# Kernel optimization log

Measured on AMD Instinct MI355X. Metric: run time of the kernel, lower is better.

The kernel has to match this reference:

```python
import jax, jax.numpy as jnp
import numpy as np

B, T, V, D = 8, 256, 32, 256


def setup_inputs() -> dict:
    key = jax.random.key(0)
    k1, k2 = jax.random.split(key)
    # scale by 0.1 so exp(q.k) stays well within fp32 range (dot std ~ 0.1^2*sqrt(D))
    feature = jax.random.normal(k1, (B, T, V, D), dtype=jnp.float32) * 0.1
    feature_aug = jax.random.normal(k2, (B, T, V, D), dtype=jnp.float32) * 0.1
    return {"feature": feature, "feature_aug": feature_aug}


def reference(feature, feature_aug):
    # match torch permute(0,2,1,3): [B,T,V,D] -> [B,V,T,D]
    f = jnp.transpose(feature, (0, 2, 1, 3))      # [B,V,Tq,D]
    fa = jnp.transpose(feature_aug, (0, 2, 1, 3))  # [B,V,Tk,D]
    # all-pairs QK^T scores: [B_i, B_j, V, Tq, Tk]
    scores = jnp.einsum('ivqd,jvkd->ijvqk', f, fa)
    E = jnp.exp(scores)
    # positive (j == i): ap = exp(scores[i,i]).sum over V, Tq -> [B, Tk]
    diag = jnp.einsum('iivqk->ivqk', E)           # [B,V,Tq,Tk]
    ap_exp = diag.sum(axis=(1, 2))                # [B, Tk]
    # negatives (j != i): sum over j,V,Tk minus the j==i part -> [B, Tq]
    total = E.sum(axis=(1, 2, 4))                 # [B, Tq]
    self_part = diag.sum(axis=(1, 3))             # [B, Tq]
    an_exp = total - self_part                    # [B, Tq]
    # per-anchor loss vector [T]; original sums over anchors then takes .mean()
    loss_vec = -jnp.log(ap_exp / an_exp)          # [B, T]
    return loss_vec.sum(axis=0).mean()
```

## Files before the change

### kernel.cpp

```cpp
#include <hip/hip_runtime.h>
#include <hip/hip_bf16.h>


typedef __attribute__((ext_vector_type(4))) float f32x4;
typedef __attribute__((ext_vector_type(4))) int   i32x4;
typedef __attribute__((ext_vector_type(8))) int   i32x8;
typedef __attribute__((ext_vector_type(8))) __bf16 bf16x8;

#if __has_builtin(__builtin_amdgcn_exp2f)
#define EXP2(x) __builtin_amdgcn_exp2f(x)
#else
#define EXP2(x) exp2f(x)
#endif

#define WAIT_VMCNT(N)                                              \
    do {                                                           \
        asm volatile("s_waitcnt vmcnt(" #N ")" ::: "memory");      \
        __builtin_amdgcn_sched_barrier(0);                         \
    } while (0)
#define WAIT_LGKM0                                                 \
    do {                                                           \
        asm volatile("s_waitcnt lgkmcnt(0)" ::: "memory");         \
        __builtin_amdgcn_sched_barrier(0);                         \
    } while (0)
#define BARRIER()                                                  \
    do {                                                           \
        __builtin_amdgcn_s_barrier();                              \
        __builtin_amdgcn_sched_barrier(0);                         \
    } while (0)

__device__ __forceinline__ unsigned short f2bf(float f) {
    unsigned u = __builtin_bit_cast(unsigned, f);
    u += 0x7FFFu + ((u >> 16) & 1u);
    return (unsigned short)(u >> 16);
}

template <bool HI>
__device__ __forceinline__ unsigned cvt2fp8(float a, float b, unsigned old) {
    return __builtin_amdgcn_cvt_pk_fp8_f32(a, b, old, HI);
}
__device__ __forceinline__ unsigned pack4fp8(float x, float y, float z, float w) {
    return cvt2fp8<true>(z, w, cvt2fp8<false>(x, y, 0u));
}

__device__ __forceinline__ void async16(const void* g, void* l) {
    __builtin_amdgcn_global_load_lds(
        (const __attribute__((address_space(1))) unsigned int*)g,
        (__attribute__((address_space(3))) unsigned int*)l,
        16, 0, 0);
}

__device__ __forceinline__ i32x8 cat8(i32x4 lo, i32x4 hi) {
    i32x8 r;
    r[0] = lo[0]; r[1] = lo[1]; r[2] = lo[2]; r[3] = lo[3];
    r[4] = hi[0]; r[5] = hi[1]; r[6] = hi[2]; r[7] = hi[3];
    return r;
}

template <int CTRL>
__device__ __forceinline__ float dpp_add(float x) {
    int y = __builtin_amdgcn_update_dpp(0, __builtin_bit_cast(int, x),
                                        CTRL, 0xf, 0xf, true);
    return x + __builtin_bit_cast(float, y);
}
__device__ __forceinline__ float rowsum16(float x) {
    x = dpp_add<0x111>(x);
    x = dpp_add<0x112>(x);
    x = dpp_add<0x114>(x);
    x = dpp_add<0x118>(x);
    return x;
}

__global__ __launch_bounds__(256) void infonce_repack_fp8(
    const float* __restrict__ feat, const float* __restrict__ feat_aug,
    unsigned char* __restrict__ pA, unsigned char* __restrict__ pB,
    float* __restrict__ counters)
{
    const int tid = threadIdx.x;
    if (blockIdx.x == 0 && blockIdx.y == 0) {
        #pragma unroll
        for (int k = 0; k < 24; ++k) counters[k * 256 + tid] = 0.f;
    }
    const bool isA = (blockIdx.y == 0);
    const float sc = isA ? 1.4426950408889634f : 1.0f;
    const float* src = isA ? feat : feat_aug;
    unsigned char* dst = isA ? pA : pB;
    const unsigned g = blockIdx.x * 256u + (unsigned)tid;
    #pragma unroll
    for (int it = 0; it < 8; ++it) {
        const unsigned idx = it * 524288u + g;
        const float4 f = *(const float4*)(src + (size_t)idx * 4);
        const unsigned p = pack4fp8(f.x * sc, f.y * sc, f.z * sc, f.w * sc);
        *(unsigned*)(dst + (size_t)idx * 4) = p;
    }
}

__global__ __launch_bounds__(256, 2) void infonce_main_nl(
    const unsigned char* __restrict__ pA, const unsigned char* __restrict__ pB,
    float* __restrict__ total, float* __restrict__ selfp, float* __restrict__ ap)
{
    __shared__ __align__(16) unsigned char As[128 * 256];
    __shared__ __align__(16) unsigned char Bs[2][64 * 256];
    float (*ls_row2)[128]  = (float (*)[128])(void*)As;
    float (*ls_self2)[128] = (float (*)[128])(void*)(As + 1024);

    const int tid  = threadIdx.x;
    const int lane = tid & 63;
    const int w    = tid >> 6;
    const int wm   = w >> 1;
    const int wn   = w & 1;
    const int lrow = lane & 15;
    const int quad = lane >> 4;

    const int tileM = blockIdx.x;
    const int v     = blockIdx.y;
    const int nD0   = (tileM >> 1) * 4;

    const size_t vOff = (size_t)v * 256;

    {
        const size_t rowM = (size_t)(tileM * 128 + w * 32 + quad) * 8192 + vOff;
        #pragma unroll
        for (int i = 0; i < 8; ++i) {
            const int lg = (lrow ^ ((i * 4 + quad) & 15)) << 4;
            async16(pA + rowM + (size_t)i * 4 * 8192 + lg, &As[(w * 32 + i * 4) * 256]);
        }
    }
    const size_t rowNbase = (size_t)(w * 16 + quad) * 8192 + vOff;
    #pragma unroll
    for (int nn = 0; nn < 2; ++nn) {
        const unsigned char* srcB = pB + rowNbase + (size_t)nn * 64 * 8192;
        #pragma unroll
        for (int i = 0; i < 4; ++i) {
            const int lg = (lrow ^ ((i * 4 + quad) & 15)) << 4;
            async16(srcB + (size_t)i * 4 * 8192 + lg,
                    &Bs[nn][(w * 16 + i * 4) * 256]);
        }
    }
    WAIT_VMCNT(4);
    BARRIER();

    i32x8 af[2][4];
    #pragma unroll
    for (int h = 0; h < 2; ++h)
        #pragma unroll
        for (int t = 0; t < 4; ++t) {
            const int rA = (wm * 64 + t * 16 + lrow) * 256;
            const int g0 = ((h * 8 + quad * 2) ^ lrow) * 16;
            af[h][t] = cat8(*(const i32x4*)&As[rA + g0],
                            *(const i32x4*)&As[rA + (g0 ^ 16)]);
        }

    float rowp[4][4];
    float selfr[4][4];
    #pragma unroll
    for (int t = 0; t < 4; ++t)
        #pragma unroll
        for (int r = 0; r < 4; ++r) { rowp[t][r] = 0.f; selfr[t][r] = 0.f; }

    auto iterBody = [&](const int n) {
        const int b = n & 1;
        BARRIER();

        i32x8 bfr[2][2];
        #pragma unroll
        for (int h = 0; h < 2; ++h)
            #pragma unroll
            for (int tj = 0; tj < 2; ++tj) {
                const int rB = (wn * 32 + tj * 16 + lrow) * 256;
                const int g0 = ((h * 8 + quad * 2) ^ lrow) * 16;
                bfr[h][tj] = cat8(*(const i32x4*)&Bs[b][rB + g0],
                                  *(const i32x4*)&Bs[b][rB + (g0 ^ 16)]);
            }
        WAIT_LGKM0;
        BARRIER();

        if (n < 30) {
            const unsigned char* src = pB + rowNbase + (size_t)(n + 2) * 64 * 8192;
            #pragma unroll
            for (int i = 0; i < 4; ++i) {
                const int lg = (lrow ^ ((i * 4 + quad) & 15)) << 4;
                async16(src + (size_t)i * 4 * 8192 + lg,
                        &Bs[b][(w * 16 + i * 4) * 256]);
            }
        }

        f32x4 acc[4][2];
        #pragma unroll
        for (int t = 0; t < 4; ++t)
            #pragma unroll
            for (int tj = 0; tj < 2; ++tj)
                acc[t][tj] = (f32x4){0.f, 0.f, 0.f, 0.f};
        __builtin_amdgcn_s_setprio(1);
        #pragma unroll
        for (int h = 0; h < 2; ++h)
            #pragma unroll
            for (int ti = 0; ti < 4; ++ti)
                #pragma unroll
                for (int tj = 0; tj < 2; ++tj)
                    acc[ti][tj] = __builtin_amdgcn_mfma_scale_f32_16x16x128_f8f6f4(
                        af[h][ti], bfr[h][tj], acc[ti][tj],
                        0, 0, 0, 127, 0, 127);
        __builtin_amdgcn_s_setprio(0);

        const bool diagIter = (n >= nD0) && (n < nD0 + 4);
        float colp0 = 0.f, colp1 = 0.f;
        #pragma unroll
        for (int t = 0; t < 4; ++t)
            #pragma unroll
            for (int r = 0; r < 4; ++r) {
                float e0 = EXP2(acc[t][0][r]);
                float e1 = EXP2(acc[t][1][r]);
                rowp[t][r] += e0 + e1;
                if (diagIter) { selfr[t][r] += e0 + e1; colp0 += e0; colp1 += e1; }
            }
        if (diagIter) {
            float q0 = colp0, q1 = colp1;
            q0 += __shfl_xor(q0, 16); q0 += __shfl_xor(q0, 32);
            q1 += __shfl_xor(q1, 16); q1 += __shfl_xor(q1, 32);
            if (lane < 16) {
                atomicAdd(&ap[n * 64 + wn * 32 + lane], q0);
                atomicAdd(&ap[n * 64 + wn * 32 + 16 + lane], q1);
            }
        }
    };

    for (int n = 0; n < 31; ++n) {
        WAIT_VMCNT(4);
        iterBody(n);
    }
    WAIT_VMCNT(0);
    iterBody(31);

    #pragma unroll
    for (int t = 0; t < 4; ++t)
        #pragma unroll
        for (int r = 0; r < 4; ++r) {
            float rs = rowsum16(rowp[t][r]);
            float ss = rowsum16(selfr[t][r]);
            if (lrow == 15) {
                const int idx = wm * 64 + t * 16 + quad * 4 + r;
                ls_row2[wn][idx]  = rs;
                ls_self2[wn][idx] = ss;
            }
        }
    __syncthreads();
    if (tid < 128) {
        atomicAdd(&total[tileM * 128 + tid], ls_row2[0][tid] + ls_row2[1][tid]);
    } else {
        const int t2 = tid - 128;
        atomicAdd(&selfp[tileM * 128 + t2], ls_self2[0][t2] + ls_self2[1][t2]);
    }
}

__global__ __launch_bounds__(256) void infonce_main_slow(
    const float* __restrict__ feat, const float* __restrict__ feat_aug,
    float* __restrict__ total, float* __restrict__ selfp, float* __restrict__ ap)
{
    __shared__ __align__(16) unsigned short As[128][72];
    __shared__ __align__(16) unsigned short Bs[128][72];
    __shared__ float ls_row[128];
    __shared__ float ls_col[128];

    const int tid  = threadIdx.x;
    const int lane = tid & 63;
    const int w    = tid >> 6;
    const int wm   = w >> 1;
    const int wn   = w & 1;
    const int lrow = lane & 15;
    const int quad = lane >> 4;

    const int tileM = blockIdx.x & 15;
    const int tileN = blockIdx.x >> 4;
    const int v     = blockIdx.y;
    const bool diag = (tileM >> 1) == (tileN >> 1);

    if (tid < 128) ls_row[tid] = 0.0f;
    else           ls_col[tid - 128] = 0.0f;

    const float* aBase = feat     + (size_t)v * 256;
    const float* bBase = feat_aug + (size_t)v * 256;

    f32x4 acc[4][4];
    #pragma unroll
    for (int i = 0; i < 4; ++i)
        #pragma unroll
        for (int j = 0; j < 4; ++j)
            acc[i][j] = (f32x4){0.f, 0.f, 0.f, 0.f};

    const int srow = tid >> 4;
    const int scol = (tid & 15) * 4;

    for (int s = 0; s < 4; ++s) {
        const int k0 = s * 64;
        if (s) __syncthreads();
        #pragma unroll
        for (int it = 0; it < 8; ++it) {
            const int row = it * 16 + srow;
            const float4 a4 = *(const float4*)(aBase + (size_t)(tileM * 128 + row) * 8192 + k0 + scol);
            const float4 b4 = *(const float4*)(bBase + (size_t)(tileN * 128 + row) * 8192 + k0 + scol);
            uint2 wa, wb;
            wa.x = (unsigned)f2bf(a4.x) | ((unsigned)f2bf(a4.y) << 16);
            wa.y = (unsigned)f2bf(a4.z) | ((unsigned)f2bf(a4.w) << 16);
            wb.x = (unsigned)f2bf(b4.x) | ((unsigned)f2bf(b4.y) << 16);
            wb.y = (unsigned)f2bf(b4.z) | ((unsigned)f2bf(b4.w) << 16);
            *(uint2*)&As[row][scol] = wa;
            *(uint2*)&Bs[row][scol] = wb;
        }
        __syncthreads();
        #pragma unroll
        for (int kk = 0; kk < 64; kk += 32) {
            bf16x8 af[4], bfr[4];
            #pragma unroll
            for (int t = 0; t < 4; ++t) {
                af[t]  = *(const bf16x8*)&As[wm * 64 + t * 16 + lrow][kk + quad * 8];
                bfr[t] = *(const bf16x8*)&Bs[wn * 64 + t * 16 + lrow][kk + quad * 8];
            }
            #pragma unroll
            for (int ti = 0; ti < 4; ++ti)
                #pragma unroll
                for (int tj = 0; tj < 4; ++tj)
                    acc[ti][tj] = __builtin_amdgcn_mfma_f32_16x16x32_bf16(
                        af[ti], bfr[tj], acc[ti][tj], 0, 0, 0);
        }
    }

    float colp[4] = {0.f, 0.f, 0.f, 0.f};
    #pragma unroll
    for (int ti = 0; ti < 4; ++ti) {
        #pragma unroll
        for (int r = 0; r < 4; ++r) {
            float e0 = __expf(acc[ti][0][r]);
            float e1 = __expf(acc[ti][1][r]);
            float e2 = __expf(acc[ti][2][r]);
            float e3 = __expf(acc[ti][3][r]);
            colp[0] += e0; colp[1] += e1; colp[2] += e2; colp[3] += e3;
            float rp = (e0 + e1) + (e2 + e3);
            rp += __shfl_xor(rp, 1);
            rp += __shfl_xor(rp, 2);
            rp += __shfl_xor(rp, 4);
            rp += __shfl_xor(rp, 8);
            if (lrow == 0)
                atomicAdd(&ls_row[wm * 64 + ti * 16 + quad * 4 + r], rp);
        }
    }
    if (diag) {
        #pragma unroll
        for (int tj = 0; tj < 4; ++tj) {
            float q = colp[tj];
            q += __shfl_xor(q, 16);
            q += __shfl_xor(q, 32);
            if (lane < 16)
                atomicAdd(&ls_col[wn * 64 + tj * 16 + lane], q);
        }
    }
    __syncthreads();
    if (tid < 128) {
        const float rs = ls_row[tid];
        const int rowg = tileM * 128 + tid;
        atomicAdd(&total[rowg], rs);
        if (diag) atomicAdd(&selfp[rowg], rs);
    } else if (diag) {
        const int t2 = tid - 128;
        atomicAdd(&ap[tileN * 128 + t2], ls_col[t2]);
    }
}

__global__ __launch_bounds__(256) void infonce_finalize(
    const float* __restrict__ total, const float* __restrict__ selfp,
    const float* __restrict__ ap, float* __restrict__ out)
{
    __shared__ float red[4];
    const int tid = threadIdx.x;
    float s = 0.f;
    for (int e = tid; e < 2048; e += 256) {
        const float an = total[e] - selfp[e];
        s += logf(an / ap[e]);
    }
    #pragma unroll
    for (int m = 32; m >= 1; m >>= 1) s += __shfl_xor(s, m);
    if ((tid & 63) == 0) red[tid >> 6] = s;
    __syncthreads();
    if (tid == 0) out[0] = (red[0] + red[1] + red[2] + red[3]) * (1.0f / 256.0f);
}

extern "C" void kernel_launch(void* const* d_in, const int* in_sizes, int n_in,
                              void* d_out, int out_size, void* d_ws, size_t ws_size,
                              hipStream_t stream) {
    const float* feat     = (const float*)d_in[0];
    const float* feat_aug = (const float*)d_in[1];
    float* total = (float*)d_ws;
    float* selfp = total + 2048;
    float* ap    = selfp + 2048;

    const size_t packBytes = (size_t)2048 * 8192;
    const size_t need = 32768 + 2 * packBytes;
    if (ws_size >= need) {
        unsigned char* pA = (unsigned char*)d_ws + 32768;
        unsigned char* pB = pA + packBytes;
        infonce_repack_fp8<<<dim3(2048, 2), 256, 0, stream>>>(feat, feat_aug, pA, pB, total);
        infonce_main_nl<<<dim3(16, 32), 256, 0, stream>>>(pA, pB, total, selfp, ap);
    } else {
        (void)hipMemsetAsync(d_ws, 0, 3 * 2048 * sizeof(float), stream);
        infonce_main_slow<<<dim3(256, 32), 256, 0, stream>>>(feat, feat_aug, total, selfp, ap);
    }
    infonce_finalize<<<1, 256, 0, stream>>>(total, selfp, ap, (float*)d_out);
}
```

Before: 189.2 us.

## Software-pipeline exp epilogue one iteration behind MFMA via ping-pong accumulators

```diff
diff --git a/kernel.cpp b/kernel.cpp
--- a/kernel.cpp
+++ b/kernel.cpp
@@ -158,8 +158,34 @@
         #pragma unroll
         for (int r = 0; r < 4; ++r) { rowp[t][r] = 0.f; selfr[t][r] = 0.f; }
 
-    auto iterBody = [&](const int n) {
+    f32x4 accA[4][2], accB[4][2];
+
+    auto epilogue = [&](const int m, f32x4 (&prev)[4][2]) {
+        const bool diagIter = (m >= nD0) && (m < nD0 + 4);
+        float colp0 = 0.f, colp1 = 0.f;
+        #pragma unroll
+        for (int t = 0; t < 4; ++t)
+            #pragma unroll
+            for (int r = 0; r < 4; ++r) {
+                float e0 = EXP2(prev[t][0][r]);
+                float e1 = EXP2(prev[t][1][r]);
+                rowp[t][r] += e0 + e1;
+                if (diagIter) { selfr[t][r] += e0 + e1; colp0 += e0; colp1 += e1; }
+            }
+        if (diagIter) {
+            float q0 = colp0, q1 = colp1;
+            q0 += __shfl_xor(q0, 16); q0 += __shfl_xor(q0, 32);
+            q1 += __shfl_xor(q1, 16); q1 += __shfl_xor(q1, 32);
+            if (lane < 16) {
+                atomicAdd(&ap[m * 64 + wn * 32 + lane], q0);
+                atomicAdd(&ap[m * 64 + wn * 32 + 16 + lane], q1);
+            }
+        }
+    };
+
+    auto step = [&](const int n, f32x4 (&cur)[4][2], f32x4 (&prev)[4][2]) {
         const int b = n & 1;
+        if (n == 31) { WAIT_VMCNT(0); } else { WAIT_VMCNT(4); }
         BARRIER();
 
         i32x8 bfr[2][2];
@@ -185,12 +211,11 @@
             }
         }
 
-        f32x4 acc[4][2];
         #pragma unroll
         for (int t = 0; t < 4; ++t)
             #pragma unroll
             for (int tj = 0; tj < 2; ++tj)
-                acc[t][tj] = (f32x4){0.f, 0.f, 0.f, 0.f};
+                cur[t][tj] = (f32x4){0.f, 0.f, 0.f, 0.f};
         __builtin_amdgcn_s_setprio(1);
         #pragma unroll
         for (int h = 0; h < 2; ++h)
@@ -198,39 +223,20 @@
             for (int ti = 0; ti < 4; ++ti)
                 #pragma unroll
                 for (int tj = 0; tj < 2; ++tj)
-                    acc[ti][tj] = __builtin_amdgcn_mfma_scale_f32_16x16x128_f8f6f4(
-                        af[h][ti], bfr[h][tj], acc[ti][tj],
+                    cur[ti][tj] = __builtin_amdgcn_mfma_scale_f32_16x16x128_f8f6f4(
+                        af[h][ti], bfr[h][tj], cur[ti][tj],
                         0, 0, 0, 127, 0, 127);
         __builtin_amdgcn_s_setprio(0);
 
-        const bool diagIter = (n >= nD0) && (n < nD0 + 4);
-        float colp0 = 0.f, colp1 = 0.f;
-        #pragma unroll
-        for (int t = 0; t < 4; ++t)
-            #pragma unroll
-            for (int r = 0; r < 4; ++r) {
-                float e0 = EXP2(acc[t][0][r]);
-                float e1 = EXP2(acc[t][1][r]);
-                rowp[t][r] += e0 + e1;
-                if (diagIter) { selfr[t][r] += e0 + e1; colp0 += e0; colp1 += e1; }
-            }
-        if (diagIter) {
-            float q0 = colp0, q1 = colp1;
-            q0 += __shfl_xor(q0, 16); q0 += __shfl_xor(q0, 32);
-            q1 += __shfl_xor(q1, 16); q1 += __shfl_xor(q1, 32);
-            if (lane < 16) {
-                atomicAdd(&ap[n * 64 + wn * 32 + lane], q0);
-                atomicAdd(&ap[n * 64 + wn * 32 + 16 + lane], q1);
-            }
-        }
+        if (n > 0) epilogue(n - 1, prev);
     };
 
-    for (int n = 0; n < 31; ++n) {
-        WAIT_VMCNT(4);
-        iterBody(n);
-    }
-    WAIT_VMCNT(0);
-    iterBody(31);
+    #pragma unroll 1
+    for (int hlf = 0; hlf < 16; ++hlf) {
+        step(2 * hlf,     accA, accB);
+        step(2 * hlf + 1, accB, accA);
+    }
+    epilogue(31, accB);
 
     #pragma unroll
     for (int t = 0; t < 4; ++t)
```

New measurement: 195.3 us. 1.03x slower.

## Fuse A-side fp8 conversion into main kernel, repack only feature_aug

Applied to the files above, without the earlier changes.

```diff
diff --git a/kernel.cpp b/kernel.cpp
--- a/kernel.cpp
+++ b/kernel.cpp
@@ -12,6 +12,8 @@
 #else
 #define EXP2(x) exp2f(x)
 #endif
+
+#define LOG2E 1.4426950408889634f
 
 #define WAIT_VMCNT(N)                                              \
     do {                                                           \
@@ -72,37 +74,32 @@
 }
 
 __global__ __launch_bounds__(256) void infonce_repack_fp8(
-    const float* __restrict__ feat, const float* __restrict__ feat_aug,
-    unsigned char* __restrict__ pA, unsigned char* __restrict__ pB,
+    const float* __restrict__ feat_aug, unsigned char* __restrict__ pB,
     float* __restrict__ counters)
 {
     const int tid = threadIdx.x;
-    if (blockIdx.x == 0 && blockIdx.y == 0) {
+    if (blockIdx.x == 0) {
         #pragma unroll
         for (int k = 0; k < 24; ++k) counters[k * 256 + tid] = 0.f;
     }
-    const bool isA = (blockIdx.y == 0);
-    const float sc = isA ? 1.4426950408889634f : 1.0f;
-    const float* src = isA ? feat : feat_aug;
-    unsigned char* dst = isA ? pA : pB;
     const unsigned g = blockIdx.x * 256u + (unsigned)tid;
     #pragma unroll
     for (int it = 0; it < 8; ++it) {
         const unsigned idx = it * 524288u + g;
-        const float4 f = *(const float4*)(src + (size_t)idx * 4);
-        const unsigned p = pack4fp8(f.x * sc, f.y * sc, f.z * sc, f.w * sc);
-        *(unsigned*)(dst + (size_t)idx * 4) = p;
+        const float4 f = *(const float4*)(feat_aug + (size_t)idx * 4);
+        const unsigned p = pack4fp8(f.x, f.y, f.z, f.w);
+        *(unsigned*)(pB + (size_t)idx * 4) = p;
     }
 }
 
 __global__ __launch_bounds__(256, 2) void infonce_main_nl(
-    const unsigned char* __restrict__ pA, const unsigned char* __restrict__ pB,
+    const float* __restrict__ feat, const unsigned char* __restrict__ pB,
     float* __restrict__ total, float* __restrict__ selfp, float* __restrict__ ap)
 {
-    __shared__ __align__(16) unsigned char As[128 * 256];
+    __shared__ __align__(16) unsigned char Stage[32 * 1024];
     __shared__ __align__(16) unsigned char Bs[2][64 * 256];
-    float (*ls_row2)[128]  = (float (*)[128])(void*)As;
-    float (*ls_self2)[128] = (float (*)[128])(void*)(As + 1024);
+    float (*ls_row2)[128]  = (float (*)[128])(void*)Stage;
+    float (*ls_self2)[128] = (float (*)[128])(void*)(Stage + 1024);
 
     const int tid  = threadIdx.x;
     const int lane = tid & 63;
@@ -118,14 +115,6 @@
 
     const size_t vOff = (size_t)v * 256;
 
-    {
-        const size_t rowM = (size_t)(tileM * 128 + w * 32 + quad) * 8192 + vOff;
-        #pragma unroll
-        for (int i = 0; i < 8; ++i) {
-            const int lg = (lrow ^ ((i * 4 + quad) & 15)) << 4;
-            async16(pA + rowM + (size_t)i * 4 * 8192 + lg, &As[(w * 32 + i * 4) * 256]);
-        }
-    }
     const size_t rowNbase = (size_t)(w * 16 + quad) * 8192 + vOff;
     #pragma unroll
     for (int nn = 0; nn < 2; ++nn) {
@@ -137,19 +126,44 @@
                     &Bs[nn][(w * 16 + i * 4) * 256]);
         }
     }
-    WAIT_VMCNT(4);
-    BARRIER();
 
     i32x8 af[2][4];
     #pragma unroll
-    for (int h = 0; h < 2; ++h)
-        #pragma unroll
-        for (int t = 0; t < 4; ++t) {
-            const int rA = (wm * 64 + t * 16 + lrow) * 256;
-            const int g0 = ((h * 8 + quad * 2) ^ lrow) * 16;
-            af[h][t] = cat8(*(const i32x4*)&As[rA + g0],
-                            *(const i32x4*)&As[rA + (g0 ^ 16)]);
-        }
+    for (int c = 0; c < 4; ++c) {
+        #pragma unroll
+        for (int i = 0; i < 8; ++i) {
+            const int rl = w * 8 + i;
+            const int gr = tileM * 128 + c * 32 + rl;
+            const int sg = lane ^ (rl & 15);
+            async16((const unsigned char*)feat +
+                        ((size_t)gr * 8192 + vOff + (size_t)sg * 4) * 4,
+                    &Stage[rl * 1024 + lane * 16]);
+        }
+        WAIT_VMCNT(0);
+        BARRIER();
+        if ((c >> 1) == wm) {
+            #pragma unroll
+            for (int tt = 0; tt < 2; ++tt) {
+                const int t  = (c & 1) * 2 + tt;
+                const int rl = tt * 16 + lrow;
+                #pragma unroll
+                for (int h = 0; h < 2; ++h) {
+                    i32x8 r;
+                    #pragma unroll
+                    for (int j = 0; j < 8; ++j) {
+                        const int G = h * 32 + quad * 8 + j;
+                        const float4 f = *(const float4*)
+                            &Stage[rl * 1024 + ((G ^ lrow) * 16)];
+                        r[j] = pack4fp8(f.x * LOG2E, f.y * LOG2E,
+                                        f.z * LOG2E, f.w * LOG2E);
+                    }
+                    af[h][t] = r;
+                }
+            }
+        }
+        WAIT_LGKM0;
+        BARRIER();
+    }
 
     float rowp[4][4];
     float selfr[4][4];
@@ -394,12 +408,11 @@
     float* ap    = selfp + 2048;
 
     const size_t packBytes = (size_t)2048 * 8192;
-    const size_t need = 32768 + 2 * packBytes;
+    const size_t need = 32768 + packBytes;
     if (ws_size >= need) {
-        unsigned char* pA = (unsigned char*)d_ws + 32768;
-        unsigned char* pB = pA + packBytes;
-        infonce_repack_fp8<<<dim3(2048, 2), 256, 0, stream>>>(feat, feat_aug, pA, pB, total);
-        infonce_main_nl<<<dim3(16, 32), 256, 0, stream>>>(pA, pB, total, selfp, ap);
+        unsigned char* pB = (unsigned char*)d_ws + 32768;
+        infonce_repack_fp8<<<dim3(2048), 256, 0, stream>>>(feat_aug, pB, total);
+        infonce_main_nl<<<dim3(16, 32), 256, 0, stream>>>(feat, pB, total, selfp, ap);
     } else {
         (void)hipMemsetAsync(d_ws, 0, 3 * 2048 * sizeof(float), stream);
         infonce_main_slow<<<dim3(256, 32), 256, 0, stream>>>(feat, feat_aug, total, selfp, ap);
```

After: 184.7 us, median of 2. -2.4%, faster.
